# Performance work log

Measured on AMD Instinct MI355X. Metric: run time of the kernel, lower is better.

Reference implementation:

```python
import jax, jax.numpy as jnp
import numpy as np

N, D, DIM, H = 50000, 32, 128, 4  # nodes, fixed degree, feature dim, heads


def setup_inputs() -> dict:
    key = jax.random.key(0)
    ks = jax.random.split(key, 8)
    s = 1.0 / np.sqrt(DIM)
    h = jax.random.normal(ks[0], (N, DIM), dtype=jnp.float32)
    neigh_idx = jax.random.randint(ks[1], (N, D), 0, N, dtype=jnp.int32)
    W = jax.random.uniform(ks[2], (H, DIM, DIM), jnp.float32, -s, s)   # per-head fciandj
    a1 = jax.random.uniform(ks[3], (H, DIM), jnp.float32, -s, s)       # key weight, src half
    a2 = jax.random.uniform(ks[4], (H, DIM), jnp.float32, -s, s)       # key weight, nbr half
    Wg = jax.random.uniform(ks[5], (DIM, H), jnp.float32, -s, s)       # GetGate projection
    W0 = jax.random.uniform(ks[6], (H * DIM, DIM), jnp.float32, -s, s) # output mix w0
    return {"h": h, "neigh_idx": neigh_idx, "W": W, "a1": a1, "a2": a2, "Wg": Wg, "W0": W0}


def reference(h, neigh_idx, W, a1, a2, Wg, W0):
    # gate per node per head (GetGate assumed: softmax over heads of linear proj)
    g = jax.nn.softmax(h @ Wg, axis=-1)            # [N, H]
    hjs = h[neigh_idx]                              # [N, D, d] per-edge gather (shared across heads)
    heads = []
    for k in range(W.shape[0]):
        wh = h @ W[k]                               # [N, d]
        whjs = jnp.einsum('ndi,ij->ndj', hjs, W[k]) # [N, D, d]
        # edge score: key([wh_i, wh_j]) = wh_i.a1 + wh_j.a2, then leaky_relu
        e = jax.nn.leaky_relu((wh @ a1[k])[:, None] + whjs @ a2[k])  # [N, D]
        att = jax.nn.softmax(e, axis=1)             # segment softmax over neighbors
        out = jax.nn.relu(jnp.einsum('nd,ndj->nj', att, whjs))       # [N, d]
        heads.append(g[:, k:k + 1] * out)
    return jnp.concatenate(heads, axis=-1) @ W0     # [N, d]
```

## Files before the change

### kernel.cpp

```cpp
#include <hip/hip_runtime.h>

typedef __attribute__((ext_vector_type(8))) short short8;
typedef __attribute__((ext_vector_type(4))) float f32x4;

__device__ __forceinline__ float bf2f(unsigned u16) {
    union { float f; unsigned u32; } v; v.u32 = u16 << 16; return v.f;
}
__device__ __forceinline__ unsigned short f2bf(float f) {
    union { float f; unsigned u32; } v; v.f = f;
    unsigned x = v.u32;
    x += ((x >> 16) & 1u) + 0x7FFFu;
    return (unsigned short)(x >> 16);
}

__global__ __launch_bounds__(256) void kprep(const float* __restrict__ W,
                                             const float* __restrict__ W0,
                                             const float* __restrict__ a1,
                                             const float* __restrict__ a2,
                                             unsigned short* __restrict__ Wt,
                                             unsigned short* __restrict__ W0t,
                                             float* __restrict__ b1,
                                             float* __restrict__ b2) {
    int b = blockIdx.x, t = threadIdx.x;
    if (b < 256) {
        int idx = b * 256 + t;
        int head = idx >> 14, rem = idx & 16383, k = rem >> 7, col = rem & 127;
        Wt[head * 16384 + col * 128 + k] = f2bf(W[idx]);
    } else if (b < 512) {
        int i2 = (b - 256) * 256 + t;
        int k = i2 >> 7, col = i2 & 127;
        W0t[col * 512 + k] = f2bf(W0[i2]);
    } else {
        int idx = (b - 512) * 256 + t;
        int k = idx >> 7, i = idx & 127;
        const float* wr = &W[k * 16384 + i * 128];
        const float* A1 = &a1[k * 128];
        const float* A2 = &a2[k * 128];
        float v1 = 0.f, v2 = 0.f;
        for (int c = 0; c < 128; ++c) { float wv = wr[c]; v1 += wv * A1[c]; v2 += wv * A2[c]; }
        b1[k * 128 + i] = v1;
        b2[k * 128 + i] = v2;
    }
}

__global__ __launch_bounds__(256) void kscore(const float* __restrict__ h,
                                              const float* __restrict__ Wg,
                                              const float* __restrict__ b1,
                                              const float* __restrict__ b2,
                                              unsigned* __restrict__ hb32,
                                              float* __restrict__ s1,
                                              float* __restrict__ s2,
                                              float* __restrict__ g,
                                              int N) {
    const int wave = threadIdx.x >> 6, lane = threadIdx.x & 63;
    const int n = blockIdx.x * 4 + wave;
    if (n >= N) return;

    float2 hv = *(const float2*)&h[(size_t)n * 128 + lane * 2];
    hb32[(size_t)n * 64 + lane] = (unsigned)f2bf(hv.x) | ((unsigned)f2bf(hv.y) << 16);

    float p[12];
    float4 wg0 = *(const float4*)&Wg[(lane * 2) * 4];
    float4 wg1 = *(const float4*)&Wg[(lane * 2 + 1) * 4];
    p[8]  = hv.x * wg0.x + hv.y * wg1.x;
    p[9]  = hv.x * wg0.y + hv.y * wg1.y;
    p[10] = hv.x * wg0.z + hv.y * wg1.z;
    p[11] = hv.x * wg0.w + hv.y * wg1.w;
    #pragma unroll
    for (int k = 0; k < 4; ++k) {
        float2 bv1 = *(const float2*)&b1[k * 128 + lane * 2];
        float2 bv2 = *(const float2*)&b2[k * 128 + lane * 2];
        p[k]     = hv.x * bv1.x + hv.y * bv1.y;
        p[4 + k] = hv.x * bv2.x + hv.y * bv2.y;
    }
    #pragma unroll
    for (int m = 32; m >= 1; m >>= 1) {
        #pragma unroll
        for (int i = 0; i < 12; ++i) p[i] += __shfl_xor(p[i], m, 64);
    }
    if (lane == 0) {
        *(float4*)&s1[n * 4] = make_float4(p[0], p[1], p[2], p[3]);
        *(float4*)&s2[n * 4] = make_float4(p[4], p[5], p[6], p[7]);
        float mx = fmaxf(fmaxf(p[8], p[9]), fmaxf(p[10], p[11]));
        float e0 = __expf(p[8] - mx), e1 = __expf(p[9] - mx);
        float e2 = __expf(p[10] - mx), e3 = __expf(p[11] - mx);
        float si = 1.f / (e0 + e1 + e2 + e3);
        *(float4*)&g[n * 4] = make_float4(e0 * si, e1 * si, e2 * si, e3 * si);
    }
}

__global__ __launch_bounds__(256) void k3_mix(const int* __restrict__ idx,
                                              const unsigned* __restrict__ hb32,
                                              const float* __restrict__ s1,
                                              const float* __restrict__ s2,
                                              unsigned* __restrict__ Mx32,
                                              int N) {
    __shared__ float att4s[4][32][4];
    const int t = threadIdx.x, w = t >> 6, l = t & 63;
    const int d = l & 31, half = l >> 5;
    int n = blockIdx.x * 4 + w;
    const bool valid = (n < N);
    if (!valid) n = N - 1;

    int j = idx[(size_t)n * 32 + d];
    float2 s2v = *(const float2*)&s2[(size_t)j * 4 + half * 2];
    const float* s1p = &s1[(size_t)n * 4];
    float e0 = s1p[half * 2] + s2v.x;
    float e1 = s1p[half * 2 + 1] + s2v.y;
    e0 = (e0 >= 0.f) ? e0 : 0.01f * e0;
    e1 = (e1 >= 0.f) ? e1 : 0.01f * e1;
    float m0 = e0, m1 = e1;
    #pragma unroll
    for (int mm = 16; mm >= 1; mm >>= 1) {
        m0 = fmaxf(m0, __shfl_xor(m0, mm, 32));
        m1 = fmaxf(m1, __shfl_xor(m1, mm, 32));
    }
    float p0 = __expf(e0 - m0), p1 = __expf(e1 - m1);
    float q0 = p0, q1 = p1;
    #pragma unroll
    for (int mm = 16; mm >= 1; mm >>= 1) {
        q0 += __shfl_xor(q0, mm, 32);
        q1 += __shfl_xor(q1, mm, 32);
    }
    *(float2*)&att4s[w][d][half * 2] = make_float2(p0 / q0, p1 / q1);

    float ac[4][2] = {};
    #pragma unroll
    for (int dd = 0; dd < 32; ++dd) {
        int jj = __shfl(j, dd, 64);
        unsigned hv = hb32[(size_t)jj * 64 + l];
        float h0 = bf2f(hv & 0xffffu);
        float h1 = bf2f(hv >> 16);
        float4 a4 = *(const float4*)&att4s[w][dd][0];
        ac[0][0] += a4.x * h0; ac[0][1] += a4.x * h1;
        ac[1][0] += a4.y * h0; ac[1][1] += a4.y * h1;
        ac[2][0] += a4.z * h0; ac[2][1] += a4.z * h1;
        ac[3][0] += a4.w * h0; ac[3][1] += a4.w * h1;
    }
    if (valid) {
        #pragma unroll
        for (int k = 0; k < 4; ++k) {
            unsigned pk = (unsigned)f2bf(ac[k][0]) | ((unsigned)f2bf(ac[k][1]) << 16);
            Mx32[(size_t)n * 256 + k * 64 + l] = pk;
        }
    }
}

typedef const __attribute__((address_space(1))) char gbyte;
typedef __attribute__((address_space(3))) char lbyte;

__global__ __launch_bounds__(512, 1) void k4_gemm(const unsigned short* __restrict__ Mx,
                                                  const unsigned short* __restrict__ Wt,
                                                  const unsigned short* __restrict__ W0t,
                                                  const float* __restrict__ g,
                                                  float* __restrict__ out,
                                                  int N, int T) {
    __shared__ unsigned short Uin[2][32 * 512];
    __shared__ unsigned short Uout[32 * 512];
    __shared__ float gld[2][128];
    const int tid = threadIdx.x, w = tid >> 6, l = tid & 63;
    const int l15 = l & 15, lh = l >> 4;
    const int hd = w & 3, ch = w >> 2;
    const int P = gridDim.x;

    short8 bf1[4][4];
    #pragma unroll
    for (int s = 0; s < 4; ++s)
        #pragma unroll
        for (int c = 0; c < 4; ++c)
            bf1[s][c] = *(const short8*)&Wt[(size_t)hd * 16384 +
                                            (size_t)((ch * 4 + c) * 16 + l15) * 128 + s * 32 + lh * 8];
    short8 bf2[16];
    #pragma unroll
    for (int ks = 0; ks < 16; ++ks)
        bf2[ks] = *(const short8*)&W0t[(size_t)(w * 16 + l15) * 512 + ks * 32 + lh * 8];

    const int t0 = blockIdx.x;

    auto STAGE = [&](int tile, int b) {
        const size_t n0 = (size_t)tile * 32;
        if (w == 0 && l < 32) {
            size_t n = n0 + l; if (n >= (size_t)N) n = N - 1;
            __builtin_amdgcn_global_load_lds((gbyte*)((const char*)g + n * 16),
                                             (lbyte*)&gld[b][0], 16, 0, 0);
        }
        #pragma unroll
        for (int p = 0; p < 4; ++p) {
            int r = p * 8 + w;
            size_t n = n0 + r;
            if (n >= (size_t)N) n = N - 1;
            const char* src = (const char*)Mx + n * 1024 + ((l * 16) ^ ((r & 7) << 4));
            __builtin_amdgcn_global_load_lds((gbyte*)src, (lbyte*)&Uin[b][r * 512], 16, 0, 0);
        }
    };

    STAGE(t0, 0);
    __syncthreads();
    if (t0 + P < T) STAGE(t0 + P, 1);

    int buf = 0;
    for (int t = t0; t < T; t += P, buf ^= 1) {
        const int n0 = t * 32;

        const char* Uibuf = (const char*)Uin[buf];
        #pragma unroll
        for (int rg = 0; rg < 2; ++rg) {
            const int arow = rg * 16 + l15;
            short8 af[4];
            #pragma unroll
            for (int s = 0; s < 4; ++s) {
                int ab = arow * 1024 + hd * 256 + s * 64 + lh * 16;
                af[s] = *(const short8*)(Uibuf + (ab ^ ((arow & 7) << 4)));
            }
            f32x4 acc[4] = {};
            #pragma unroll
            for (int s = 0; s < 4; ++s)
                #pragma unroll
                for (int c = 0; c < 4; ++c)
                    acc[c] = __builtin_amdgcn_mfma_f32_16x16x32_bf16(af[s], bf1[s][c], acc[c], 0, 0, 0);
            #pragma unroll
            for (int c = 0; c < 4; ++c) {
                const int col = hd * 128 + (ch * 4 + c) * 16 + l15;
                #pragma unroll
                for (int r = 0; r < 4; ++r) {
                    int row = rg * 16 + lh * 4 + r;
                    float v = fmaxf(acc[c][r], 0.f) * gld[buf][row * 4 + hd];
                    int ub = row * 1024 + col * 2;
                    *(unsigned short*)((char*)Uout + (ub ^ ((row & 7) << 4))) = f2bf(v);
                }
            }
        }

        __syncthreads();

        if (t + 2 * P < T) STAGE(t + 2 * P, buf);

        const char* Uob = (const char*)Uout;
        #pragma unroll
        for (int rg = 0; rg < 2; ++rg) {
            const int arow = rg * 16 + l15;
            f32x4 oacc = {};
            #pragma unroll
            for (int ks = 0; ks < 16; ++ks) {
                int ab = arow * 1024 + ks * 64 + lh * 16;
                short8 afr = *(const short8*)(Uob + (ab ^ ((arow & 7) << 4)));
                oacc = __builtin_amdgcn_mfma_f32_16x16x32_bf16(afr, bf2[ks], oacc, 0, 0, 0);
            }
            #pragma unroll
            for (int r = 0; r < 4; ++r) {
                int n = n0 + rg * 16 + lh * 4 + r;
                if (n < N) out[(size_t)n * 128 + w * 16 + l15] = oacc[r];
            }
        }

        __syncthreads();
    }
}

extern "C" void kernel_launch(void* const* d_in, const int* in_sizes, int n_in,
                              void* d_out, int out_size, void* d_ws, size_t ws_size,
                              hipStream_t stream) {
    const float* h     = (const float*)d_in[0];
    const int*   neigh = (const int*)d_in[1];
    const float* W     = (const float*)d_in[2];
    const float* a1    = (const float*)d_in[3];
    const float* a2    = (const float*)d_in[4];
    const float* Wg    = (const float*)d_in[5];
    const float* W0    = (const float*)d_in[6];
    float* out = (float*)d_out;

    const int N = in_sizes[0] / 128;

    char* ws = (char*)d_ws;
    unsigned* hb32 = (unsigned*)ws;
    unsigned* Mx32 = (unsigned*)(ws + (size_t)N * 256);
    float* s1 = (float*)(ws + (size_t)N * 256 + (size_t)N * 1024);
    float* s2 = s1 + (size_t)N * 4;
    float* g  = s2 + (size_t)N * 4;
    unsigned short* Wt  = (unsigned short*)(g + (size_t)N * 4);
    unsigned short* W0t = Wt + 65536;
    float* b1 = (float*)(W0t + 65536);
    float* b2 = b1 + 512;

    const int T = (N + 31) / 32;
    const int P = (T < 256) ? T : 256;

    kprep<<<dim3(514), dim3(256), 0, stream>>>(W, W0, a1, a2, Wt, W0t, b1, b2);
    kscore<<<dim3((N + 3) / 4), dim3(256), 0, stream>>>(h, Wg, b1, b2, hb32, s1, s2, g, N);
    k3_mix<<<dim3((N + 3) / 4), dim3(256), 0, stream>>>(neigh, hb32, s1, s2, Mx32, N);
    k4_gemm<<<dim3(P), dim3(512), 0, stream>>>((const unsigned short*)Mx32, Wt, W0t, g,
                                               out, N, T);
}
```

Before: 138.0 us.

## Fuse neighbor aggregation into GEMM kernel and widen score kernel per-thread work

```diff
diff --git a/kernel.cpp b/kernel.cpp
--- a/kernel.cpp
+++ b/kernel.cpp
@@ -11,6 +11,9 @@
     unsigned x = v.u32;
     x += ((x >> 16) & 1u) + 0x7FFFu;
     return (unsigned short)(x >> 16);
+}
+__device__ __forceinline__ unsigned packbf(float a, float b) {
+    return (unsigned)f2bf(a) | ((unsigned)f2bf(b) << 16);
 }
 
 __global__ __launch_bounds__(256) void kprep(const float* __restrict__ W,
@@ -52,33 +55,47 @@
                                               float* __restrict__ s2,
                                               float* __restrict__ g,
                                               int N) {
-    const int wave = threadIdx.x >> 6, lane = threadIdx.x & 63;
-    const int n = blockIdx.x * 4 + wave;
+    const int t = threadIdx.x, w = t >> 6, l = t & 63;
+    const int grp = l >> 4, q = l & 15;
+    const int n = blockIdx.x * 16 + w * 4 + grp;
     if (n >= N) return;
 
-    float2 hv = *(const float2*)&h[(size_t)n * 128 + lane * 2];
-    hb32[(size_t)n * 64 + lane] = (unsigned)f2bf(hv.x) | ((unsigned)f2bf(hv.y) << 16);
+    float4 hv0 = *(const float4*)&h[(size_t)n * 128 + q * 8];
+    float4 hv1 = *(const float4*)&h[(size_t)n * 128 + q * 8 + 4];
+    float ha[8] = {hv0.x, hv0.y, hv0.z, hv0.w, hv1.x, hv1.y, hv1.z, hv1.w};
+
+    uint4 hbv;
+    hbv.x = packbf(ha[0], ha[1]); hbv.y = packbf(ha[2], ha[3]);
+    hbv.z = packbf(ha[4], ha[5]); hbv.w = packbf(ha[6], ha[7]);
+    *(uint4*)&hb32[(size_t)n * 64 + q * 4] = hbv;
 
     float p[12];
-    float4 wg0 = *(const float4*)&Wg[(lane * 2) * 4];
-    float4 wg1 = *(const float4*)&Wg[(lane * 2 + 1) * 4];
-    p[8]  = hv.x * wg0.x + hv.y * wg1.x;
-    p[9]  = hv.x * wg0.y + hv.y * wg1.y;
-    p[10] = hv.x * wg0.z + hv.y * wg1.z;
-    p[11] = hv.x * wg0.w + hv.y * wg1.w;
     #pragma unroll
     for (int k = 0; k < 4; ++k) {
-        float2 bv1 = *(const float2*)&b1[k * 128 + lane * 2];
-        float2 bv2 = *(const float2*)&b2[k * 128 + lane * 2];
-        p[k]     = hv.x * bv1.x + hv.y * bv1.y;
-        p[4 + k] = hv.x * bv2.x + hv.y * bv2.y;
-    }
-    #pragma unroll
-    for (int m = 32; m >= 1; m >>= 1) {
-        #pragma unroll
-        for (int i = 0; i < 12; ++i) p[i] += __shfl_xor(p[i], m, 64);
-    }
-    if (lane == 0) {
+        float4 ba = *(const float4*)&b1[k * 128 + q * 8];
+        float4 bb = *(const float4*)&b1[k * 128 + q * 8 + 4];
+        p[k] = ha[0]*ba.x + ha[1]*ba.y + ha[2]*ba.z + ha[3]*ba.w
+             + ha[4]*bb.x + ha[5]*bb.y + ha[6]*bb.z + ha[7]*bb.w;
+        float4 ca = *(const float4*)&b2[k * 128 + q * 8];
+        float4 cb = *(const float4*)&b2[k * 128 + q * 8 + 4];
+        p[4+k] = ha[0]*ca.x + ha[1]*ca.y + ha[2]*ca.z + ha[3]*ca.w
+               + ha[4]*cb.x + ha[5]*cb.y + ha[6]*cb.z + ha[7]*cb.w;
+    }
+    p[8] = p[9] = p[10] = p[11] = 0.f;
+    #pragma unroll
+    for (int e = 0; e < 8; ++e) {
+        float4 wg = *(const float4*)&Wg[(q * 8 + e) * 4];
+        p[8]  += ha[e] * wg.x;
+        p[9]  += ha[e] * wg.y;
+        p[10] += ha[e] * wg.z;
+        p[11] += ha[e] * wg.w;
+    }
+    #pragma unroll
+    for (int m = 8; m >= 1; m >>= 1) {
+        #pragma unroll
+        for (int i = 0; i < 12; ++i) p[i] += __shfl_xor(p[i], m, 16);
+    }
+    if (q == 0) {
         *(float4*)&s1[n * 4] = make_float4(p[0], p[1], p[2], p[3]);
         *(float4*)&s2[n * 4] = make_float4(p[4], p[5], p[6], p[7]);
         float mx = fmaxf(fmaxf(p[8], p[9]), fmaxf(p[10], p[11]));
@@ -89,78 +106,22 @@
     }
 }
 
-__global__ __launch_bounds__(256) void k3_mix(const int* __restrict__ idx,
-                                              const unsigned* __restrict__ hb32,
-                                              const float* __restrict__ s1,
-                                              const float* __restrict__ s2,
-                                              unsigned* __restrict__ Mx32,
-                                              int N) {
-    __shared__ float att4s[4][32][4];
-    const int t = threadIdx.x, w = t >> 6, l = t & 63;
-    const int d = l & 31, half = l >> 5;
-    int n = blockIdx.x * 4 + w;
-    const bool valid = (n < N);
-    if (!valid) n = N - 1;
-
-    int j = idx[(size_t)n * 32 + d];
-    float2 s2v = *(const float2*)&s2[(size_t)j * 4 + half * 2];
-    const float* s1p = &s1[(size_t)n * 4];
-    float e0 = s1p[half * 2] + s2v.x;
-    float e1 = s1p[half * 2 + 1] + s2v.y;
-    e0 = (e0 >= 0.f) ? e0 : 0.01f * e0;
-    e1 = (e1 >= 0.f) ? e1 : 0.01f * e1;
-    float m0 = e0, m1 = e1;
-    #pragma unroll
-    for (int mm = 16; mm >= 1; mm >>= 1) {
-        m0 = fmaxf(m0, __shfl_xor(m0, mm, 32));
-        m1 = fmaxf(m1, __shfl_xor(m1, mm, 32));
-    }
-    float p0 = __expf(e0 - m0), p1 = __expf(e1 - m1);
-    float q0 = p0, q1 = p1;
-    #pragma unroll
-    for (int mm = 16; mm >= 1; mm >>= 1) {
-        q0 += __shfl_xor(q0, mm, 32);
-        q1 += __shfl_xor(q1, mm, 32);
-    }
-    *(float2*)&att4s[w][d][half * 2] = make_float2(p0 / q0, p1 / q1);
-
-    float ac[4][2] = {};
-    #pragma unroll
-    for (int dd = 0; dd < 32; ++dd) {
-        int jj = __shfl(j, dd, 64);
-        unsigned hv = hb32[(size_t)jj * 64 + l];
-        float h0 = bf2f(hv & 0xffffu);
-        float h1 = bf2f(hv >> 16);
-        float4 a4 = *(const float4*)&att4s[w][dd][0];
-        ac[0][0] += a4.x * h0; ac[0][1] += a4.x * h1;
-        ac[1][0] += a4.y * h0; ac[1][1] += a4.y * h1;
-        ac[2][0] += a4.z * h0; ac[2][1] += a4.z * h1;
-        ac[3][0] += a4.w * h0; ac[3][1] += a4.w * h1;
-    }
-    if (valid) {
-        #pragma unroll
-        for (int k = 0; k < 4; ++k) {
-            unsigned pk = (unsigned)f2bf(ac[k][0]) | ((unsigned)f2bf(ac[k][1]) << 16);
-            Mx32[(size_t)n * 256 + k * 64 + l] = pk;
-        }
-    }
-}
-
-typedef const __attribute__((address_space(1))) char gbyte;
-typedef __attribute__((address_space(3))) char lbyte;
-
-__global__ __launch_bounds__(512, 1) void k4_gemm(const unsigned short* __restrict__ Mx,
-                                                  const unsigned short* __restrict__ Wt,
-                                                  const unsigned short* __restrict__ W0t,
-                                                  const float* __restrict__ g,
-                                                  float* __restrict__ out,
-                                                  int N, int T) {
-    __shared__ unsigned short Uin[2][32 * 512];
+__global__ __launch_bounds__(512, 1) void kfused(const int* __restrict__ idx,
+                                                 const unsigned* __restrict__ hb32,
+                                                 const float* __restrict__ s1,
+                                                 const float* __restrict__ s2,
+                                                 const float* __restrict__ g,
+                                                 const unsigned short* __restrict__ Wt,
+                                                 const unsigned short* __restrict__ W0t,
+                                                 float* __restrict__ out,
+                                                 int N, int T) {
+    __shared__ unsigned short Uin[32 * 512];
     __shared__ unsigned short Uout[32 * 512];
-    __shared__ float gld[2][128];
+    __shared__ float att4s[8][32][4];
     const int tid = threadIdx.x, w = tid >> 6, l = tid & 63;
     const int l15 = l & 15, lh = l >> 4;
     const int hd = w & 3, ch = w >> 2;
+    const int d = l & 31, half = l >> 5;
     const int P = gridDim.x;
 
     short8 bf1[4][4];
@@ -175,34 +136,69 @@
     for (int ks = 0; ks < 16; ++ks)
         bf2[ks] = *(const short8*)&W0t[(size_t)(w * 16 + l15) * 512 + ks * 32 + lh * 8];
 
-    const int t0 = blockIdx.x;
-
-    auto STAGE = [&](int tile, int b) {
-        const size_t n0 = (size_t)tile * 32;
-        if (w == 0 && l < 32) {
-            size_t n = n0 + l; if (n >= (size_t)N) n = N - 1;
-            __builtin_amdgcn_global_load_lds((gbyte*)((const char*)g + n * 16),
-                                             (lbyte*)&gld[b][0], 16, 0, 0);
+    for (int t = blockIdx.x; t < T; t += P) {
+        const int n0 = t * 32;
+
+        float gv[2][4];
+        #pragma unroll
+        for (int rg = 0; rg < 2; ++rg)
+            #pragma unroll
+            for (int r = 0; r < 4; ++r) {
+                int n = n0 + rg * 16 + lh * 4 + r;
+                gv[rg][r] = (n < N) ? g[(size_t)n * 4 + hd] : 0.f;
+            }
+
+        #pragma unroll
+        for (int i = 0; i < 4; ++i) {
+            const int row = w * 4 + i;
+            int n = n0 + row;
+            if (n >= N) n = N - 1;
+
+            int j = idx[(size_t)n * 32 + d];
+            float2 s2v = *(const float2*)&s2[(size_t)j * 4 + half * 2];
+            float2 s1v = *(const float2*)&s1[(size_t)n * 4 + half * 2];
+            float e0 = s1v.x + s2v.x;
+            float e1 = s1v.y + s2v.y;
+            e0 = (e0 >= 0.f) ? e0 : 0.01f * e0;
+            e1 = (e1 >= 0.f) ? e1 : 0.01f * e1;
+            float m0 = e0, m1 = e1;
+            #pragma unroll
+            for (int mm = 16; mm >= 1; mm >>= 1) {
+                m0 = fmaxf(m0, __shfl_xor(m0, mm, 32));
+                m1 = fmaxf(m1, __shfl_xor(m1, mm, 32));
+            }
+            float p0 = __expf(e0 - m0), p1 = __expf(e1 - m1);
+            float q0 = p0, q1 = p1;
+            #pragma unroll
+            for (int mm = 16; mm >= 1; mm >>= 1) {
+                q0 += __shfl_xor(q0, mm, 32);
+                q1 += __shfl_xor(q1, mm, 32);
+            }
+            *(float2*)&att4s[w][d][half * 2] = make_float2(p0 / q0, p1 / q1);
+
+            float ac[4][2] = {};
+            #pragma unroll
+            for (int dd = 0; dd < 32; ++dd) {
+                int jj = __shfl(j, dd, 64);
+                unsigned hv = hb32[(size_t)jj * 64 + l];
+                float h0 = bf2f(hv & 0xffffu);
+                float h1 = bf2f(hv >> 16);
+                float4 a4 = *(const float4*)&att4s[w][dd][0];
+                ac[0][0] += a4.x * h0; ac[0][1] += a4.x * h1;
+                ac[1][0] += a4.y * h0; ac[1][1] += a4.y * h1;
+                ac[2][0] += a4.z * h0; ac[2][1] += a4.z * h1;
+                ac[3][0] += a4.w * h0; ac[3][1] += a4.w * h1;
+            }
+            const int base = row * 1024 + l * 4;
+            #pragma unroll
+            for (int k = 0; k < 4; ++k) {
+                unsigned pk = packbf(ac[k][0], ac[k][1]);
+                *(unsigned*)((char*)Uin + ((base + k * 256) ^ ((row & 7) << 4))) = pk;
+            }
         }
-        #pragma unroll
-        for (int p = 0; p < 4; ++p) {
-            int r = p * 8 + w;
-            size_t n = n0 + r;
-            if (n >= (size_t)N) n = N - 1;
-            const char* src = (const char*)Mx + n * 1024 + ((l * 16) ^ ((r & 7) << 4));
-            __builtin_amdgcn_global_load_lds((gbyte*)src, (lbyte*)&Uin[b][r * 512], 16, 0, 0);
-        }
-    };
-
-    STAGE(t0, 0);
-    __syncthreads();
-    if (t0 + P < T) STAGE(t0 + P, 1);
-
-    int buf = 0;
-    for (int t = t0; t < T; t += P, buf ^= 1) {
-        const int n0 = t * 32;
-
-        const char* Uibuf = (const char*)Uin[buf];
+        __syncthreads();
+
+        const char* Uib = (const char*)Uin;
         #pragma unroll
         for (int rg = 0; rg < 2; ++rg) {
             const int arow = rg * 16 + l15;
@@ -210,7 +206,7 @@
             #pragma unroll
             for (int s = 0; s < 4; ++s) {
                 int ab = arow * 1024 + hd * 256 + s * 64 + lh * 16;
-                af[s] = *(const short8*)(Uibuf + (ab ^ ((arow & 7) << 4)));
+                af[s] = *(const short8*)(Uib + (ab ^ ((arow & 7) << 4)));
             }
             f32x4 acc[4] = {};
             #pragma unroll
@@ -224,16 +220,13 @@
                 #pragma unroll
                 for (int r = 0; r < 4; ++r) {
                     int row = rg * 16 + lh * 4 + r;
-                    float v = fmaxf(acc[c][r], 0.f) * gld[buf][row * 4 + hd];
+                    float v = fmaxf(acc[c][r], 0.f) * gv[rg][r];
                     int ub = row * 1024 + col * 2;
                     *(unsigned short*)((char*)Uout + (ub ^ ((row & 7) << 4))) = f2bf(v);
                 }
             }
         }
-
         __syncthreads();
-
-        if (t + 2 * P < T) STAGE(t + 2 * P, buf);
 
         const char* Uob = (const char*)Uout;
         #pragma unroll
@@ -252,7 +245,6 @@
                 if (n < N) out[(size_t)n * 128 + w * 16 + l15] = oacc[r];
             }
         }
-
         __syncthreads();
     }
 }
@@ -273,7 +265,6 @@
 
     char* ws = (char*)d_ws;
     unsigned* hb32 = (unsigned*)ws;
-    unsigned* Mx32 = (unsigned*)(ws + (size_t)N * 256);
     float* s1 = (float*)(ws + (size_t)N * 256 + (size_t)N * 1024);
     float* s2 = s1 + (size_t)N * 4;
     float* g  = s2 + (size_t)N * 4;
@@ -283,11 +274,9 @@
     float* b2 = b1 + 512;
 
     const int T = (N + 31) / 32;
-    const int P = (T < 256) ? T : 256;
+    const int P = (T < 512) ? T : 512;
 
     kprep<<<dim3(514), dim3(256), 0, stream>>>(W, W0, a1, a2, Wt, W0t, b1, b2);
-    kscore<<<dim3((N + 3) / 4), dim3(256), 0, stream>>>(h, Wg, b1, b2, hb32, s1, s2, g, N);
-    k3_mix<<<dim3((N + 3) / 4), dim3(256), 0, stream>>>(neigh, hb32, s1, s2, Mx32, N);
-    k4_gemm<<<dim3(P), dim3(512), 0, stream>>>((const unsigned short*)Mx32, Wt, W0t, g,
-                                               out, N, T);
-}
+    kscore<<<dim3((N + 15) / 16), dim3(256), 0, stream>>>(h, Wg, b1, b2, hb32, s1, s2, g, N);
+    kfused<<<dim3(P), dim3(512), 0, stream>>>(neigh, hb32, s1, s2, g, Wt, W0t, out, N, T);
+}
```

After: 511.6 us. 3.71x slower.
